# Optimization experiments

Measured on AMD Instinct MI355X. Metric: run time of the kernel, lower is better.

## Reference

```python
import jax, jax.numpy as jnp
import numpy as np

BATCH, PAST_N, HID, FEAT = 256, 512, 512, 1
INIT_MULT = 0.01  # ones * 0.01 initial state (perturb_init=False / eval mode)


def setup_inputs() -> dict:
    key = jax.random.key(0)
    ks = jax.random.split(key, 8)
    s = 1.0 / np.sqrt(HID)
    return {
        "input_seq": jax.random.normal(ks[0], (BATCH, PAST_N, FEAT), dtype=jnp.float32),
        "future_n": 64,
        "W_ih": jax.random.uniform(ks[1], (4 * HID, FEAT), minval=-s, maxval=s, dtype=jnp.float32),
        "W_hh": jax.random.uniform(ks[2], (4 * HID, HID), minval=-s, maxval=s, dtype=jnp.float32),
        "b_ih": jax.random.uniform(ks[3], (4 * HID,), minval=-s, maxval=s, dtype=jnp.float32),
        "b_hh": jax.random.uniform(ks[4], (4 * HID,), minval=-s, maxval=s, dtype=jnp.float32),
        "W_dec": jax.random.uniform(ks[5], (FEAT, HID), minval=-s, maxval=s, dtype=jnp.float32),
        "b_dec": jax.random.uniform(ks[6], (FEAT,), minval=-s, maxval=s, dtype=jnp.float32),
    }


def _lstm_cell(x, h, c, W_ih, W_hh, b_ih, b_hh):
    # PyTorch LSTMCell: gates ordered (i, f, g, o)
    gates = x @ W_ih.T + b_ih + h @ W_hh.T + b_hh  # [B, 4H]
    i, f, g, o = jnp.split(gates, 4, axis=-1)
    c_new = jax.nn.sigmoid(f) * c + jax.nn.sigmoid(i) * jnp.tanh(g)
    h_new = jax.nn.sigmoid(o) * jnp.tanh(c_new)
    return h_new, c_new


def reference(input_seq, future_n, W_ih, W_hh, b_ih, b_hh, W_dec, b_dec):
    B, T, _ = input_seq.shape
    h0 = jnp.full((B, HID), INIT_MULT, dtype=input_seq.dtype)
    c0 = jnp.full((B, HID), INIT_MULT, dtype=input_seq.dtype)

    xs = jnp.swapaxes(input_seq, 0, 1)  # [T, B, F]

    def past_step(carry, x_t):
        h, c = carry
        h, c = _lstm_cell(x_t, h, c, W_ih, W_hh, b_ih, b_hh)
        return (h, c), h

    (h, c), past_h = jax.lax.scan(past_step, (h0, c0), xs)  # past_h: [T, B, H]

    def future_step(carry, _):
        h, c = carry
        x_t = h @ W_dec.T + b_dec  # decode hidden -> next input, [B, F]
        h, c = _lstm_cell(x_t, h, c, W_ih, W_hh, b_ih, b_hh)
        return (h, c), h

    _, fut_h = jax.lax.scan(future_step, (h, c), None, length=future_n)  # [F_n, B, H]

    all_h = jnp.concatenate([past_h, fut_h], axis=0)  # [T+F_n, B, H]
    all_h = jnp.swapaxes(all_h, 0, 1)  # [B, T+F_n, H]
    return all_h @ W_dec.T + b_dec  # [B, T+F_n, 1]
```

## Files before the change

kernel.cpp:

```cpp
#include <hip/hip_runtime.h>
#include <hip/hip_fp16.h>


#define TPAST 512
#define TTOT  576
#define HIDN  512
#define BW    16
#define HW    64
#define NGRP  8
#define NWG   128
#define NTHR  512
#define HSTR  520
#define GSTR  261
#define BATCHN 256

typedef _Float16 half8   __attribute__((ext_vector_type(8)));
typedef _Float16 half2v  __attribute__((ext_vector_type(2)));
typedef float    float4v __attribute__((ext_vector_type(4)));
typedef int      int4v   __attribute__((ext_vector_type(4)));

__device__ __forceinline__ float fast_exp(float x) {
    return __builtin_amdgcn_exp2f(x * 1.44269504f);
}
__device__ __forceinline__ float fast_sigmoid(float x) {
    return __builtin_amdgcn_rcpf(1.0f + fast_exp(-x));
}
__device__ __forceinline__ float fast_tanh(float x) {
    return 1.0f - 2.0f * __builtin_amdgcn_rcpf(fast_exp(2.0f * x) + 1.0f);
}

__device__ __forceinline__ void ld32_sys(const void* p, int4v& a, int4v& b) {
    asm volatile("global_load_dwordx4 %0, %2, off sc0 sc1\n\t"
                 "global_load_dwordx4 %1, %2, off offset:16 sc0 sc1\n\t"
                 "s_waitcnt vmcnt(0)"
                 : "=v"(a), "=v"(b) : "v"(p) : "memory");
}
__device__ __forceinline__ void drain_vm() {
    asm volatile("s_waitcnt vmcnt(0)" ::: "memory");
}

__global__ __launch_bounds__(NTHR, 1)
void lstm_forecast_kernel(const float* __restrict__ xseq,
                          const float* __restrict__ Wih,
                          const float* __restrict__ Whh,
                          const float* __restrict__ bih,
                          const float* __restrict__ bhh,
                          const float* __restrict__ Wdec,
                          const float* __restrict__ bdec,
                          float* __restrict__ out,
                          unsigned int* __restrict__ flagbase,
                          unsigned int* __restrict__ hbuf)
{
    __shared__ _Float16 hcur[BW * HSTR];
    __shared__ float    gates[BW * GSTR];
    __shared__ float    wdecs[HIDN];
    __shared__ float    xcur[BW];

    const int tid  = threadIdx.x;
    const int bb   = blockIdx.x & 15;
    const int gb   = blockIdx.x >> 4;
    const int lane = tid & 63;
    const int wave = tid >> 6;
    const int m    = lane & 15;
    const int q    = lane >> 4;

    half8 Wf[2][16];
    {
        #pragma unroll
        for (int cbi = 0; cbi < 2; ++cbi) {
            const int col = (2 * wave + cbi) * 16 + m;
            const int gt  = col >> 6;
            const int jl  = col & 63;
            const float* wr = Whh + (size_t)(gt * HIDN + gb * HW + jl) * HIDN;
            #pragma unroll
            for (int kk = 0; kk < 16; ++kk) {
                const int k0 = kk * 32 + q * 8;
                float4v u = *(const float4v*)(wr + k0);
                float4v v = *(const float4v*)(wr + k0 + 4);
                half8 h;
                h[0] = (_Float16)u[0]; h[1] = (_Float16)u[1];
                h[2] = (_Float16)u[2]; h[3] = (_Float16)u[3];
                h[4] = (_Float16)v[0]; h[5] = (_Float16)v[1];
                h[6] = (_Float16)v[2]; h[7] = (_Float16)v[3];
                Wf[cbi][kk] = h;
            }
        }
    }

    const int eb = tid >> 5;
    const int jj = tid & 31;
    const int j0 = 2 * jj;
    float wih_r[2][4], bsum_r[2][4];
    #pragma unroll
    for (int p = 0; p < 2; ++p) {
        const int jg = gb * HW + j0 + p;
        #pragma unroll
        for (int gt = 0; gt < 4; ++gt) {
            const int r = gt * HIDN + jg;
            wih_r[p][gt]  = Wih[r];
            bsum_r[p][gt] = bih[r] + bhh[r];
        }
    }
    const float bdecv = bdec[0];
    float c0 = 0.01f, c1 = 0.01f;

    {
        const _Float16 hinit = (_Float16)0.01f;
        for (int i = tid; i < BW * HSTR; i += NTHR) hcur[i] = hinit;
        wdecs[tid] = Wdec[tid];
        if (tid < BW) xcur[tid] = xseq[(bb * BW + tid) * TPAST + 0];
    }
    __syncthreads();

    unsigned int* gflags = flagbase + bb * 16;
    const int bglob_e = bb * BW + eb;

    for (int t = 0; t < TTOT; ++t) {
        float4v acc0 = {0.f, 0.f, 0.f, 0.f};
        float4v acc1 = {0.f, 0.f, 0.f, 0.f};
        const _Float16* arow = hcur + m * HSTR + q * 8;
        #pragma unroll
        for (int kk = 0; kk < 16; ++kk) {
            half8 af = *(const half8*)(arow + kk * 32);
            acc0 = __builtin_amdgcn_mfma_f32_16x16x32_f16(af, Wf[0][kk], acc0, 0, 0, 0);
            acc1 = __builtin_amdgcn_mfma_f32_16x16x32_f16(af, Wf[1][kk], acc1, 0, 0, 0);
        }
        {
            const int colbase = wave * 32;
            #pragma unroll
            for (int r = 0; r < 4; ++r) {
                gates[(q * 4 + r) * GSTR + colbase +      m] = acc0[r];
                gates[(q * 4 + r) * GSTR + colbase + 16 + m] = acc1[r];
            }
        }
        const int tn = t + 1;
        float xq = 0.f;
        if (tn < TPAST && tid < BW) xq = xseq[(bb * BW + tid) * TPAST + tn];

        __syncthreads();

        {
            const float xc = xcur[eb];
            const float* grow = gates + eb * GSTR;

            float gi = grow[       j0] + xc * wih_r[0][0] + bsum_r[0][0];
            float gf = grow[ 64  + j0] + xc * wih_r[0][1] + bsum_r[0][1];
            float gg = grow[128  + j0] + xc * wih_r[0][2] + bsum_r[0][2];
            float go = grow[192  + j0] + xc * wih_r[0][3] + bsum_r[0][3];
            c0 = fast_sigmoid(gf) * c0 + fast_sigmoid(gi) * fast_tanh(gg);
            const float h0 = fast_sigmoid(go) * fast_tanh(c0);

            gi = grow[       j0 + 1] + xc * wih_r[1][0] + bsum_r[1][0];
            gf = grow[ 64  + j0 + 1] + xc * wih_r[1][1] + bsum_r[1][1];
            gg = grow[128  + j0 + 1] + xc * wih_r[1][2] + bsum_r[1][2];
            go = grow[192  + j0 + 1] + xc * wih_r[1][3] + bsum_r[1][3];
            c1 = fast_sigmoid(gf) * c1 + fast_sigmoid(gi) * fast_tanh(gg);
            const float h1 = fast_sigmoid(go) * fast_tanh(c1);

            half2v hp; hp[0] = (_Float16)h0; hp[1] = (_Float16)h1;

            *(half2v*)(hcur + eb * HSTR + gb * HW + j0) = hp;

            const unsigned int bits = __builtin_bit_cast(unsigned int, hp);
            unsigned int* hdst = hbuf
                + (size_t)((tn & 1) * BATCHN + bglob_e) * (HIDN / 2)
                + gb * (HW / 2) + jj;
            __hip_atomic_store(hdst, bits, __ATOMIC_RELAXED,
                               __HIP_MEMORY_SCOPE_AGENT);
        }

        drain_vm();
        __syncthreads();

        const unsigned int target = (unsigned int)tn;
        if (wave == gb && lane == 0)
            __hip_atomic_store(gflags + gb, target, __ATOMIC_RELAXED,
                               __HIP_MEMORY_SCOPE_AGENT);
        if (wave != gb) {
            const unsigned int* slot = gflags + wave;
            int guard = 0;
            for (;;) {
                const unsigned int v = __hip_atomic_load(
                    slot, __ATOMIC_RELAXED, __HIP_MEMORY_SCOPE_AGENT);
                if (v >= target) break;
                __builtin_amdgcn_s_sleep(1);
                if (++guard > (1 << 22)) break;
            }
            __builtin_amdgcn_sched_barrier(0);

            const int p1 = tn & 1;
            const char* src = (const char*)hbuf
                + ((size_t)(p1 * BATCHN + bb * BW)) * (HIDN * 2)
                + (size_t)(lane >> 2) * (HIDN * 2)
                + wave * (HW * 2)
                + (lane & 3) * 32;
            int4v a, b;
            ld32_sys(src, a, b);
            _Float16* dst = hcur + (lane >> 2) * HSTR + wave * HW
                            + (lane & 3) * 16;
            *(int4v*)(dst)     = a;
            *(int4v*)(dst + 8) = b;
        }
        __syncthreads();

        if (wave < 2) {
            const int brow = 2 * gb + wave;
            const _Float16* hr = hcur + brow * HSTR + lane * 8;
            const float*    wr = wdecs + lane * 8;
            half8 hv = *(const half8*)hr;
            float dx = 0.f;
            #pragma unroll
            for (int e = 0; e < 8; ++e) dx += (float)hv[e] * wr[e];
            dx += __shfl_down(dx, 32);
            dx += __shfl_down(dx, 16);
            dx += __shfl_down(dx, 8);
            dx += __shfl_down(dx, 4);
            dx += __shfl_down(dx, 2);
            dx += __shfl_down(dx, 1);
            if (lane == 0)
                out[(bb * BW + brow) * TTOT + t] = dx + bdecv;
        }
        if (tn >= TPAST) {
            const _Float16* hr = hcur + eb * HSTR + jj * 16;
            const float*    wr = wdecs + jj * 16;
            float dx = 0.f;
            #pragma unroll
            for (int u = 0; u < 2; ++u) {
                half8 hv = *(const half8*)(hr + u * 8);
                #pragma unroll
                for (int e = 0; e < 8; ++e)
                    dx += (float)hv[e] * wr[u * 8 + e];
            }
            dx += __shfl_down(dx, 16);
            dx += __shfl_down(dx, 8);
            dx += __shfl_down(dx, 4);
            dx += __shfl_down(dx, 2);
            dx += __shfl_down(dx, 1);
            if ((lane & 31) == 0) xcur[eb] = dx + bdecv;
        } else {
            if (tid < BW) xcur[tid] = xq;
        }
    }
}

extern "C" void kernel_launch(void* const* d_in, const int* in_sizes, int n_in,
                              void* d_out, int out_size, void* d_ws, size_t ws_size,
                              hipStream_t stream) {
    (void)in_sizes; (void)n_in; (void)ws_size; (void)out_size;
    const float* xseq = (const float*)d_in[0];
    const float* Wih  = (const float*)d_in[2];
    const float* Whh  = (const float*)d_in[3];
    const float* bih  = (const float*)d_in[4];
    const float* bhh  = (const float*)d_in[5];
    const float* Wdec = (const float*)d_in[6];
    const float* bdec = (const float*)d_in[7];
    float* out = (float*)d_out;

    unsigned int* flags = (unsigned int*)d_ws;
    unsigned int* hbuf  = (unsigned int*)((char*)d_ws + 8192);

    hipMemsetAsync(d_ws, 0, 8192, stream);
    lstm_forecast_kernel<<<dim3(NWG), dim3(NTHR), 0, stream>>>(
        xseq, Wih, Whh, bih, bhh, Wdec, bdec, out, flags, hbuf);
}
```

Baseline: 1.669 ms.

## Replace flag-based handoff with tag bits embedded in fp32 hidden-state words

Removes the per-group flag variable, the vmcnt drain and the extra block barrier before signalling. Each hidden value is now stored as fp32 with its low mantissa bit replaced by a step-parity tag, so consumers poll the data itself until every word carries the expected tag, then convert to fp16. This shortens the signal-then-read round trip to a single polled load path. In exchange it doubles the exchanged bytes, adds conversion work and two buffer memsets, and relies on 64-bit stores being seen atomically.

```diff
diff --git a/kernel.cpp b/kernel.cpp
--- a/kernel.cpp
+++ b/kernel.cpp
@@ -7,7 +7,6 @@
 #define HIDN  512
 #define BW    16
 #define HW    64
-#define NGRP  8
 #define NWG   128
 #define NTHR  512
 #define HSTR  520
@@ -29,14 +28,14 @@
     return 1.0f - 2.0f * __builtin_amdgcn_rcpf(fast_exp(2.0f * x) + 1.0f);
 }
 
-__device__ __forceinline__ void ld32_sys(const void* p, int4v& a, int4v& b) {
-    asm volatile("global_load_dwordx4 %0, %2, off sc0 sc1\n\t"
-                 "global_load_dwordx4 %1, %2, off offset:16 sc0 sc1\n\t"
+__device__ __forceinline__ void ld64_sys(const void* p, int4v& a, int4v& b,
+                                         int4v& c, int4v& d) {
+    asm volatile("global_load_dwordx4 %0, %4, off sc0 sc1\n\t"
+                 "global_load_dwordx4 %1, %4, off offset:16 sc0 sc1\n\t"
+                 "global_load_dwordx4 %2, %4, off offset:32 sc0 sc1\n\t"
+                 "global_load_dwordx4 %3, %4, off offset:48 sc0 sc1\n\t"
                  "s_waitcnt vmcnt(0)"
-                 : "=v"(a), "=v"(b) : "v"(p) : "memory");
-}
-__device__ __forceinline__ void drain_vm() {
-    asm volatile("s_waitcnt vmcnt(0)" ::: "memory");
+                 : "=v"(a), "=v"(b), "=v"(c), "=v"(d) : "v"(p) : "memory");
 }
 
 __global__ __launch_bounds__(NTHR, 1)
@@ -48,7 +47,6 @@
                           const float* __restrict__ Wdec,
                           const float* __restrict__ bdec,
                           float* __restrict__ out,
-                          unsigned int* __restrict__ flagbase,
                           unsigned int* __restrict__ hbuf)
 {
     __shared__ _Float16 hcur[BW * HSTR];
@@ -112,7 +110,6 @@
     }
     __syncthreads();
 
-    unsigned int* gflags = flagbase + bb * 16;
     const int bglob_e = bb * BW + eb;
 
     for (int t = 0; t < TTOT; ++t) {
@@ -134,6 +131,7 @@
             }
         }
         const int tn = t + 1;
+        const unsigned int tag = ((unsigned int)tn >> 1) & 1u;
         float xq = 0.f;
         if (tn < TPAST && tid < BW) xq = xseq[(bb * BW + tid) * TPAST + tn];
 
@@ -158,48 +156,73 @@
             const float h1 = fast_sigmoid(go) * fast_tanh(c1);
 
             half2v hp; hp[0] = (_Float16)h0; hp[1] = (_Float16)h1;
-
             *(half2v*)(hcur + eb * HSTR + gb * HW + j0) = hp;
 
-            const unsigned int bits = __builtin_bit_cast(unsigned int, hp);
-            unsigned int* hdst = hbuf
-                + (size_t)((tn & 1) * BATCHN + bglob_e) * (HIDN / 2)
-                + gb * (HW / 2) + jj;
-            __hip_atomic_store(hdst, bits, __ATOMIC_RELAXED,
+            const unsigned int u0 =
+                (__builtin_bit_cast(unsigned int, h0) & ~1u) | tag;
+            const unsigned int u1 =
+                (__builtin_bit_cast(unsigned int, h1) & ~1u) | tag;
+            const unsigned long long uv =
+                ((unsigned long long)u1 << 32) | (unsigned long long)u0;
+            unsigned long long* hdst = (unsigned long long*)
+                (hbuf + (size_t)((tn & 1) * BATCHN + bglob_e) * HIDN
+                      + gb * HW + j0);
+            __hip_atomic_store(hdst, uv, __ATOMIC_RELAXED,
                                __HIP_MEMORY_SCOPE_AGENT);
         }
 
-        drain_vm();
-        __syncthreads();
-
-        const unsigned int target = (unsigned int)tn;
-        if (wave == gb && lane == 0)
-            __hip_atomic_store(gflags + gb, target, __ATOMIC_RELAXED,
-                               __HIP_MEMORY_SCOPE_AGENT);
         if (wave != gb) {
-            const unsigned int* slot = gflags + wave;
+            const int p1 = tn & 1;
+            const int r  = lane >> 2;
+            const int c4 = lane & 3;
+            const unsigned int* src = hbuf
+                + (size_t)(p1 * BATCHN + bb * BW + r) * HIDN
+                + wave * HW + c4 * 16;
+            int4v a, b, c, d;
             int guard = 0;
-            for (;;) {
-                const unsigned int v = __hip_atomic_load(
-                    slot, __ATOMIC_RELAXED, __HIP_MEMORY_SCOPE_AGENT);
-                if (v >= target) break;
-                __builtin_amdgcn_s_sleep(1);
-                if (++guard > (1 << 22)) break;
+            if (tag) {
+                for (;;) {
+                    ld64_sys(src, a, b, c, d);
+                    const unsigned int x =
+                        (unsigned int)((a[0] & a[1] & a[2] & a[3]) &
+                                       (b[0] & b[1] & b[2] & b[3]) &
+                                       (c[0] & c[1] & c[2] & c[3]) &
+                                       (d[0] & d[1] & d[2] & d[3]));
+                    if (__ballot((x & 1u) != 0u) == ~0ull) break;
+                    __builtin_amdgcn_s_sleep(1);
+                    if (++guard > (1 << 20)) break;
+                }
+            } else {
+                for (;;) {
+                    ld64_sys(src, a, b, c, d);
+                    const unsigned int x =
+                        (unsigned int)((a[0] | a[1] | a[2] | a[3]) |
+                                       (b[0] | b[1] | b[2] | b[3]) |
+                                       (c[0] | c[1] | c[2] | c[3]) |
+                                       (d[0] | d[1] | d[2] | d[3]));
+                    if (__ballot((x & 1u) == 0u) == ~0ull) break;
+                    __builtin_amdgcn_s_sleep(1);
+                    if (++guard > (1 << 20)) break;
+                }
             }
             __builtin_amdgcn_sched_barrier(0);
 
-            const int p1 = tn & 1;
-            const char* src = (const char*)hbuf
-                + ((size_t)(p1 * BATCHN + bb * BW)) * (HIDN * 2)
-                + (size_t)(lane >> 2) * (HIDN * 2)
-                + wave * (HW * 2)
-                + (lane & 3) * 32;
-            int4v a, b;
-            ld32_sys(src, a, b);
-            _Float16* dst = hcur + (lane >> 2) * HSTR + wave * HW
-                            + (lane & 3) * 16;
-            *(int4v*)(dst)     = a;
-            *(int4v*)(dst + 8) = b;
+            const float4v fa = __builtin_bit_cast(float4v, a);
+            const float4v fb = __builtin_bit_cast(float4v, b);
+            const float4v fc = __builtin_bit_cast(float4v, c);
+            const float4v fd = __builtin_bit_cast(float4v, d);
+            half8 hlo, hhi;
+            hlo[0] = (_Float16)fa[0]; hlo[1] = (_Float16)fa[1];
+            hlo[2] = (_Float16)fa[2]; hlo[3] = (_Float16)fa[3];
+            hlo[4] = (_Float16)fb[0]; hlo[5] = (_Float16)fb[1];
+            hlo[6] = (_Float16)fb[2]; hlo[7] = (_Float16)fb[3];
+            hhi[0] = (_Float16)fc[0]; hhi[1] = (_Float16)fc[1];
+            hhi[2] = (_Float16)fc[2]; hhi[3] = (_Float16)fc[3];
+            hhi[4] = (_Float16)fd[0]; hhi[5] = (_Float16)fd[1];
+            hhi[6] = (_Float16)fd[2]; hhi[7] = (_Float16)fd[3];
+            _Float16* dst = hcur + r * HSTR + wave * HW + c4 * 16;
+            *(half8*)dst       = hlo;
+            *(half8*)(dst + 8) = hhi;
         }
         __syncthreads();
 
@@ -256,10 +279,11 @@
     const float* bdec = (const float*)d_in[7];
     float* out = (float*)d_out;
 
-    unsigned int* flags = (unsigned int*)d_ws;
-    unsigned int* hbuf  = (unsigned int*)((char*)d_ws + 8192);
-
-    hipMemsetAsync(d_ws, 0, 8192, stream);
+    unsigned int* hbuf = (unsigned int*)d_ws;
+    const size_t half_bytes = (size_t)BATCHN * HIDN * 4;
+
+    hipMemsetAsync(hbuf, 0x00, half_bytes, stream);
+    hipMemsetAsync((char*)hbuf + half_bytes, 0xFF, half_bytes, stream);
     lstm_forecast_kernel<<<dim3(NWG), dim3(NTHR), 0, stream>>>(
-        xseq, Wih, Whh, bih, bhh, Wdec, bdec, out, flags, hbuf);
-}
+        xseq, Wih, Whh, bih, bhh, Wdec, bdec, out, hbuf);
+}
```

Result: slower. 2.543 ms (+52.4%).

## Centralize cross-workgroup flag polling in one wave and relax hidden-state loads

Applied to the files above, without the earlier changes.

Instead of each of the seven remote waves polling its own global flag, the wave that owns this workgroup's slice polls all eight flags in parallel lanes and uses a ballot to detect completion, then publishes a go signal through LDS that the other waves spin on. The hidden-state gather switches from system-scope (sc0 sc1) 32-byte loads to agent-scope (sc1) 16-byte loads with a more coalesced row layout. This is meant to cut global polling traffic and load latency per timestep, at the cost of an extra LDS handoff hop and weaker cache-coherence bits that must still see peer workgroups' writes.

```diff
diff --git a/kernel.cpp b/kernel.cpp
--- a/kernel.cpp
+++ b/kernel.cpp
@@ -7,7 +7,6 @@
 #define HIDN  512
 #define BW    16
 #define HW    64
-#define NGRP  8
 #define NWG   128
 #define NTHR  512
 #define HSTR  520
@@ -29,11 +28,10 @@
     return 1.0f - 2.0f * __builtin_amdgcn_rcpf(fast_exp(2.0f * x) + 1.0f);
 }
 
-__device__ __forceinline__ void ld32_sys(const void* p, int4v& a, int4v& b) {
-    asm volatile("global_load_dwordx4 %0, %2, off sc0 sc1\n\t"
-                 "global_load_dwordx4 %1, %2, off offset:16 sc0 sc1\n\t"
+__device__ __forceinline__ void ld16_agent(const void* p, int4v& a) {
+    asm volatile("global_load_dwordx4 %0, %1, off sc1\n\t"
                  "s_waitcnt vmcnt(0)"
-                 : "=v"(a), "=v"(b) : "v"(p) : "memory");
+                 : "=v"(a) : "v"(p) : "memory");
 }
 __device__ __forceinline__ void drain_vm() {
     asm volatile("s_waitcnt vmcnt(0)" ::: "memory");
@@ -55,6 +53,7 @@
     __shared__ float    gates[BW * GSTR];
     __shared__ float    wdecs[HIDN];
     __shared__ float    xcur[BW];
+    __shared__ unsigned int go_lds;
 
     const int tid  = threadIdx.x;
     const int bb   = blockIdx.x & 15;
@@ -109,6 +108,7 @@
         for (int i = tid; i < BW * HSTR; i += NTHR) hcur[i] = hinit;
         wdecs[tid] = Wdec[tid];
         if (tid < BW) xcur[tid] = xseq[(bb * BW + tid) * TPAST + 0];
+        if (tid == 0) go_lds = 0;
     }
     __syncthreads();
 
@@ -173,33 +173,45 @@
         __syncthreads();
 
         const unsigned int target = (unsigned int)tn;
-        if (wave == gb && lane == 0)
+        if (tid == 0)
             __hip_atomic_store(gflags + gb, target, __ATOMIC_RELAXED,
                                __HIP_MEMORY_SCOPE_AGENT);
-        if (wave != gb) {
-            const unsigned int* slot = gflags + wave;
+
+        if (wave == gb) {
+            const unsigned int* slot = gflags + (lane & 7);
+            const bool own = (lane & 7) == gb;
             int guard = 0;
             for (;;) {
                 const unsigned int v = __hip_atomic_load(
                     slot, __ATOMIC_RELAXED, __HIP_MEMORY_SCOPE_AGENT);
-                if (v >= target) break;
+                if (__ballot(own || v >= target) == ~0ull) break;
+                __builtin_amdgcn_s_sleep(1);
+                if (++guard > (1 << 20)) break;
+            }
+            __hip_atomic_store(&go_lds, target, __ATOMIC_RELAXED,
+                               __HIP_MEMORY_SCOPE_WORKGROUP);
+        } else {
+            int guard = 0;
+            while (__hip_atomic_load(&go_lds, __ATOMIC_RELAXED,
+                                     __HIP_MEMORY_SCOPE_WORKGROUP) < target) {
                 __builtin_amdgcn_s_sleep(1);
                 if (++guard > (1 << 22)) break;
             }
             __builtin_amdgcn_sched_barrier(0);
 
             const int p1 = tn & 1;
-            const char* src = (const char*)hbuf
+            const char* base = (const char*)hbuf
                 + ((size_t)(p1 * BATCHN + bb * BW)) * (HIDN * 2)
-                + (size_t)(lane >> 2) * (HIDN * 2)
                 + wave * (HW * 2)
-                + (lane & 3) * 32;
+                + (lane & 7) * 16;
+            const int r0 = lane >> 3;
             int4v a, b;
-            ld32_sys(src, a, b);
-            _Float16* dst = hcur + (lane >> 2) * HSTR + wave * HW
-                            + (lane & 3) * 16;
-            *(int4v*)(dst)     = a;
-            *(int4v*)(dst + 8) = b;
+            ld16_agent(base + (size_t)r0 * (HIDN * 2), a);
+            ld16_agent(base + (size_t)(r0 + 8) * (HIDN * 2), b);
+            _Float16* dst0 = hcur + r0 * HSTR + wave * HW + (lane & 7) * 8;
+            _Float16* dst1 = dst0 + 8 * HSTR;
+            *(int4v*)dst0 = a;
+            *(int4v*)dst1 = b;
         }
         __syncthreads();
 
```

Result: slower. 1.785 ms (+7.0%).
